# Optimization experiments

Measured on AMD Instinct MI355X. Metric: run time of the kernel, lower is better.

Reference implementation:

```python
import jax, jax.numpy as jnp
from jax import lax
import numpy as np

ROI = 7  # roi_size


def _extract_rois(feat, coords):
    """Faithful port of extract_roi_features: clamp a 7x7 window to image bounds,
    then bilinearly resize the (possibly smaller) crop back to 7x7
    (F.interpolate, mode='bilinear', align_corners=False)."""
    B, C, H, W = feat.shape
    half = ROI // 2

    def axis_idx(c, size):
        start = jnp.maximum(0, c - half)                  # [B,A]
        end = jnp.minimum(size, c + half + 1)
        Li = end - start                                  # crop length (int) [B,A]
        L = Li.astype(feat.dtype)[..., None]              # [B,A,1]
        j = jnp.arange(ROI, dtype=feat.dtype)
        # align_corners=False source coordinate, clamped into the crop
        src = jnp.clip((j + 0.5) * L / ROI - 0.5, 0.0, L - 1.0)  # [B,A,7]
        i0 = jnp.floor(src).astype(jnp.int32)
        i1 = jnp.minimum(i0 + 1, Li[..., None] - 1)
        w1 = src - i0.astype(feat.dtype)
        return start[..., None] + i0, start[..., None] + i1, 1.0 - w1, w1

    xc = coords[..., 0].astype(jnp.int32)
    yc = coords[..., 1].astype(jnp.int32)
    y0, y1, wy0, wy1 = axis_idx(yc, H)
    x0, x1, wx0, wx1 = axis_idx(xc, W)
    Bn, A = xc.shape
    bi = jnp.arange(Bn)[:, None, None, None]

    def g(Y, X):  # gather -> [B,A,7,7,C]
        return feat[bi, :, Y[:, :, :, None], X[:, :, None, :]]

    wy0 = wy0[:, :, :, None, None]; wy1 = wy1[:, :, :, None, None]
    wx0 = wx0[:, :, None, :, None]; wx1 = wx1[:, :, None, :, None]
    v = (wy0 * wx0 * g(y0, x0) + wy0 * wx1 * g(y0, x1)
         + wy1 * wx0 * g(y1, x0) + wy1 * wx1 * g(y1, x1))
    return jnp.transpose(v, (0, 1, 4, 2, 3))  # [B,A,C,7,7]


def _conv(x, w, b, pad):
    y = lax.conv_general_dilated(x, w, (1, 1), [(pad, pad), (pad, pad)],
                                 dimension_numbers=('NCHW', 'OIHW', 'NCHW'))
    return y + b[None, :, None, None]


def _bn(x, scale, bias, mean, var, eps=1e-5):
    inv = scale * lax.rsqrt(var + eps)
    return x * inv[None, :, None, None] + (bias - mean * inv)[None, :, None, None]


def setup_inputs() -> dict:
    key = jax.random.key(0)
    ks = jax.random.split(key, 12)
    B, A, C, H, W = 8, 128, 256, 64, 64
    f32 = jnp.float32
    d = {}
    d['feat_rgb'] = jax.random.normal(ks[0], (B, C, H, W), f32)
    d['feat_tir'] = jax.random.normal(ks[1], (B, C, H, W), f32)
    d['anchor_coords'] = jax.random.randint(ks[2], (B, A, 2), 0, 64).astype(jnp.int32)
    # local_fusion: Conv(2C->C,3) BN ReLU Conv(C->C,3) BN ReLU
    d['conv1_w'] = jax.random.normal(ks[3], (C, 2 * C, 3, 3), f32) * 0.02
    d['conv1_b'] = jnp.zeros((C,), f32)
    d['bn1_scale'] = jnp.ones((C,), f32)
    d['bn1_bias'] = jnp.zeros((C,), f32)
    d['bn1_mean'] = jax.random.normal(ks[4], (C,), f32) * 0.1
    d['bn1_var'] = jax.random.uniform(ks[5], (C,), f32, 0.5, 1.5)
    d['conv2_w'] = jax.random.normal(ks[6], (C, C, 3, 3), f32) * 0.02
    d['conv2_b'] = jnp.zeros((C,), f32)
    d['bn2_scale'] = jnp.ones((C,), f32)
    d['bn2_bias'] = jnp.zeros((C,), f32)
    d['bn2_mean'] = jax.random.normal(ks[7], (C,), f32) * 0.1
    d['bn2_var'] = jax.random.uniform(ks[8], (C,), f32, 0.5, 1.5)
    # weight_generator: Conv(C->C//4,1) ReLU Conv(C//4->2,1) Softmax(dim=1)
    d['wg1_w'] = jax.random.normal(ks[9], (C // 4, C, 1, 1), f32) * 0.05
    d['wg1_b'] = jnp.zeros((C // 4,), f32)
    d['wg2_w'] = jax.random.normal(ks[10], (2, C // 4, 1, 1), f32) * 0.05
    d['wg2_b'] = jnp.zeros((2,), f32)
    return d


def reference(feat_rgb, feat_tir, anchor_coords,
              conv1_w, conv1_b, bn1_scale, bn1_bias, bn1_mean, bn1_var,
              conv2_w, conv2_b, bn2_scale, bn2_bias, bn2_mean, bn2_var,
              wg1_w, wg1_b, wg2_w, wg2_b):
    B, C, H, W = feat_rgb.shape
    A = anchor_coords.shape[1]
    roi_rgb = _extract_rois(feat_rgb, anchor_coords)  # [B,A,C,7,7]
    roi_tir = _extract_rois(feat_tir, anchor_coords)
    rgb = roi_rgb.reshape(B * A, C, ROI, ROI)
    tir = roi_tir.reshape(B * A, C, ROI, ROI)
    x = jnp.concatenate([rgb, tir], axis=1)           # [B*A, 2C, 7, 7]
    x = jax.nn.relu(_bn(_conv(x, conv1_w, conv1_b, 1), bn1_scale, bn1_bias, bn1_mean, bn1_var))
    x = jax.nn.relu(_bn(_conv(x, conv2_w, conv2_b, 1), bn2_scale, bn2_bias, bn2_mean, bn2_var))
    h = jax.nn.relu(_conv(x, wg1_w, wg1_b, 0))
    w = jax.nn.softmax(_conv(h, wg2_w, wg2_b, 0), axis=1)  # [B*A, 2, 7, 7]
    fused = w[:, 0:1] * rgb + w[:, 1:2] * tir
    return fused.reshape(B, A, C, ROI, ROI)
```

## Files before the change

kernel.cpp:

```cpp
#include <hip/hip_runtime.h>
#include <cstddef>
#include <cstdint>


typedef unsigned int u32;
typedef unsigned short u16;
typedef __attribute__((ext_vector_type(8))) short short8;
typedef __attribute__((ext_vector_type(16))) float float16v;

__device__ __forceinline__ float bf2f(u16 u) {
  u32 x = ((u32)u) << 16;
  return __builtin_bit_cast(float, x);
}
__device__ __forceinline__ u16 f2bf(float f) {
  u32 x = __builtin_bit_cast(u32, f);
  x = x + 0x7fffu + ((x >> 16) & 1u);
  return (u16)(x >> 16);
}
__device__ __forceinline__ void gl_lds16(const void* g, void* l) {
  __builtin_amdgcn_global_load_lds((const __attribute__((address_space(1))) void*)g,
                                   (__attribute__((address_space(3))) void*)l, 16, 0, 0);
}

template <int IC>
__global__ void k_prep_w(const float* __restrict__ w, u16* __restrict__ wt) {
  int i = blockIdx.x * 256 + threadIdx.x;
  if (i >= 9 * 256 * IC) return;
  int e = i & 7;
  int r = i >> 3;
  int oc = r & 255;
  int r2 = r >> 8;
  int oct = r2 % (IC / 8);
  int t = r2 / (IC / 8);
  int ic = oct * 8 + e;
  wt[i] = f2bf(w[((size_t)oc * IC + ic) * 9 + t]);
}

__global__ void k_prep_bn(const float* __restrict__ cb, const float* __restrict__ sc,
                          const float* __restrict__ bi, const float* __restrict__ mn,
                          const float* __restrict__ vr, float* __restrict__ sb,
                          float* __restrict__ zp) {
  int c = threadIdx.x;
  float inv = sc[c] * rsqrtf(vr[c] + 1e-5f);
  sb[c]       = inv;
  sb[256 + c] = cb[c] * inv + (bi[c] - mn[c] * inv);
  zp[c] = 0.0f;
  zp[256 + c] = 0.0f;
}

__global__ __launch_bounds__(256)
void k_roi2(const float* __restrict__ frgb, const float* __restrict__ ftir,
            const int* __restrict__ coords, u16* __restrict__ cat) {
  int ba = blockIdx.x, b = ba >> 7, tid = threadIdx.x;
  __shared__ int   si0[2][7], si1[2][7];
  __shared__ float sw0[2][7], sw1[2][7];
  __shared__ u16 tile[49][514];
  if (tid < 14) {
    int axis = tid / 7;
    int j = tid - axis * 7;
    int c = coords[ba * 2 + (axis == 0 ? 1 : 0)];
    int start = max(0, c - 3);
    int end   = min(64, c + 4);
    int Li = end - start;
    float L = (float)Li;
    float src = ((float)j + 0.5f) * L / 7.0f - 0.5f;
    src = fminf(fmaxf(src, 0.0f), L - 1.0f);
    int i0 = (int)floorf(src);
    int i1 = min(i0 + 1, Li - 1);
    float w1 = src - (float)i0;
    si0[axis][j] = start + i0;
    si1[axis][j] = start + i1;
    sw0[axis][j] = 1.0f - w1;
    sw1[axis][j] = w1;
  }
  __syncthreads();
  const float* fr = frgb + (size_t)b * 256 * 4096;
  const float* ft = ftir + (size_t)b * 256 * 4096;
  for (int idx = tid; idx < 256 * 49; idx += 256) {
    int c = idx / 49, p = idx - c * 49;
    int jy = p / 7, jx = p - (p / 7) * 7;
    int y0 = si0[0][jy], y1 = si1[0][jy];
    int x0 = si0[1][jx], x1 = si1[1][jx];
    float wy0 = sw0[0][jy], wy1 = sw1[0][jy];
    float wx0 = sw0[1][jx], wx1 = sw1[1][jx];
    float a00 = wy0 * wx0, a01 = wy0 * wx1, a10 = wy1 * wx0, a11 = wy1 * wx1;
    const float* fc = fr + (size_t)c * 4096;
    float vr_ = a00 * fc[y0 * 64 + x0] + a01 * fc[y0 * 64 + x1] +
                a10 * fc[y1 * 64 + x0] + a11 * fc[y1 * 64 + x1];
    const float* gc = ft + (size_t)c * 4096;
    float vt_ = a00 * gc[y0 * 64 + x0] + a01 * gc[y0 * 64 + x1] +
                a10 * gc[y1 * 64 + x0] + a11 * gc[y1 * 64 + x1];
    tile[p][c]       = f2bf(vr_);
    tile[p][256 + c] = f2bf(vt_);
  }
  __syncthreads();
  u16* dst = cat + (size_t)ba * 49 * 512;
  for (int o = tid; o < 49 * 512; o += 256) {
    int row = o >> 9, c = o & 511;
    dst[o] = tile[row][c];
  }
}

template <int ICT, bool FIRST>
__global__ __launch_bounds__(1024, 4)
void k_conv_mfma(const u16* __restrict__ IN, const u16* __restrict__ WT,
                 const float* __restrict__ sb, const float* __restrict__ zpad,
                 u16* __restrict__ OUT) {
  constexpr int NC = ICT / 64;
  constexpr int BUFB = 208 * 128;
  __shared__ __align__(16) u16 lds[3][BUFB / 2];
  const int tid = threadIdx.x;
  const int lane = tid & 63, wv = tid >> 6;
  const int ng = wv & 3, mg = wv >> 2;
  const int l31 = lane & 31, h32 = lane >> 5;
  const int ba4 = blockIdx.x * 4;
  const char* inb = (const char*)IN;
  const char* zpb = (const char*)zpad;
  const bool dead1 = (mg == 3);

  int base_[2], qy_[2], qx_[2];
#pragma unroll
  for (int i = 0; i < 2; ++i) {
    int P = (mg + 4 * i) * 32 + l31;
    if (P > 195) P = 195;
    int roi = P / 49;
    int q = P - roi * 49;
    base_[i] = roi * 49;
    qy_[i] = q / 7;
    qx_[i] = q - (q / 7) * 7;
  }

  float16v acc[2][2];
#pragma unroll
  for (int i = 0; i < 2; ++i)
#pragma unroll
    for (int f = 0; f < 2; ++f)
#pragma unroll
      for (int e = 0; e < 16; ++e) acc[i][f][e] = 0.0f;

  auto stage = [&](int ch, int buf) {
    int cl = ((lane & 7) * 16) ^ (((lane >> 3) & 7) << 4);
#pragma unroll
    for (int u = 0; u < 2; ++u) {
      int s = wv + u * 16;
      int soff = (s <= 24) ? s * 1024 : 25 * 1024;
      int row_g = s * 8 + (lane >> 3);
      const char* src = (row_g < 196)
          ? (inb + ((size_t)(ba4 * 49 + row_g)) * (ICT * 2) + ch * 128 + cl)
          : (zpb + cl);
      gl_lds16(src, (char*)&lds[buf][0] + soff);
    }
  };

  const u16* wthr = WT + (size_t)h32 * 2048 + (size_t)(ng * 64 + l31) * 8;

  stage(0, 0);
  stage(1, 1);
  asm volatile("s_waitcnt vmcnt(2)" ::: "memory");
  __builtin_amdgcn_sched_barrier(0);
  __builtin_amdgcn_s_barrier();
  __builtin_amdgcn_sched_barrier(0);

#pragma unroll 1
  for (int ch = 0; ch < NC; ++ch) {
    if (ch + 2 < NC) stage(ch + 2, (ch + 2) % 3);
    const char* lb = (const char*)&lds[ch % 3][0];
    const u16* wch = wthr + (size_t)ch * 8 * 2048;

    short8 wfr[3][2];
#pragma unroll
    for (int jp = 0; jp < 2; ++jp)
#pragma unroll
      for (int f = 0; f < 2; ++f)
        wfr[jp][f] = *(const short8*)(
            wch + (size_t)(jp * 2) * 2048 + f * 256);
    int row0 = 0, row1 = 0;
#pragma unroll
    for (int j = 0; j < 36; ++j) {
      const int t = j >> 2, kk = j & 3;
      if (kk == 0) {
        const int dy = t / 3 - 1, dx = t - (t / 3) * 3 - 1;
#pragma unroll
        for (int i = 0; i < 2; ++i) {
          int iy = qy_[i] + dy, ix = qx_[i] + dx;
          int ok = ((u32)iy < 7u) & ((u32)ix < 7u);
          int row = ok ? (base_[i] + iy * 7 + ix) : 196;
          if (i == 0) row0 = row; else row1 = row;
        }
      }
      if (j + 2 < 36) {
        const int jn = j + 2;
#pragma unroll
        for (int f = 0; f < 2; ++f)
          wfr[jn % 3][f] = *(const short8*)(
              wch + (size_t)((jn >> 2) * (ICT / 8) + (jn & 3) * 2) * 2048 + f * 256);
      }
      short8 bfr[2];
      {
        int byt0 = row0 * 128 + ((kk * 32 + h32 * 16) ^ ((row0 & 7) << 4));
        bfr[0] = *(const short8*)(lb + byt0);
      }
      if (!dead1) {
        int byt1 = row1 * 128 + ((kk * 32 + h32 * 16) ^ ((row1 & 7) << 4));
        bfr[1] = *(const short8*)(lb + byt1);
      }
      __builtin_amdgcn_s_setprio(1);
#pragma unroll
      for (int i = 0; i < 2; ++i) {
        if (i == 1 && dead1) continue;
#pragma unroll
        for (int f = 0; f < 2; ++f)
          acc[i][f] = FIRST
              ? __builtin_amdgcn_mfma_f32_32x32x16_bf16(bfr[i], wfr[j % 3][f],
                                                        acc[i][f], 0, 0, 0)
              : __builtin_amdgcn_mfma_f32_32x32x16_bf16(wfr[j % 3][f], bfr[i],
                                                        acc[i][f], 0, 0, 0);
      }
      __builtin_amdgcn_s_setprio(0);
    }

    if (ch + 2 < NC) {
      asm volatile("s_waitcnt vmcnt(2)" ::: "memory");
    } else {
      asm volatile("s_waitcnt vmcnt(0)" ::: "memory");
    }
    __builtin_amdgcn_sched_barrier(0);
    __builtin_amdgcn_s_barrier();
    __builtin_amdgcn_sched_barrier(0);
  }

  if (FIRST) {
    u16* ob = OUT + (size_t)ba4 * 49 * 256;
#pragma unroll
    for (int f = 0; f < 2; ++f) {
      int oc = ng * 64 + f * 32 + l31;
      float s = sb[oc], bb = sb[256 + oc];
#pragma unroll
      for (int i = 0; i < 2; ++i) {
        if (i == 1 && dead1) continue;
        int ti = mg + 4 * i;
#pragma unroll
        for (int reg = 0; reg < 16; ++reg) {
          int m = (reg & 3) + 8 * (reg >> 2) + 4 * h32;
          int P = ti * 32 + m;
          if (P < 196)
            ob[(size_t)P * 256 + oc] = f2bf(fmaxf(acc[i][f][reg] * s + bb, 0.0f));
        }
      }
    }
  } else {
#pragma unroll
    for (int i = 0; i < 2; ++i) {
      if (i == 1 && dead1) continue;
      int ti = mg + 4 * i;
      int P = ti * 32 + l31;
      if (P < 196) {
        int roi = P / 49;
        int q = P - roi * 49;
        u16* ob = OUT + ((size_t)(ba4 + roi) * 256) * 49 + q;
#pragma unroll
        for (int f = 0; f < 2; ++f)
#pragma unroll
          for (int reg = 0; reg < 16; ++reg) {
            int oc = ng * 64 + f * 32 + (reg & 3) + 8 * (reg >> 2) + 4 * h32;
            float s = sb[oc], bb = sb[256 + oc];
            ob[(size_t)oc * 49] = f2bf(fmaxf(acc[i][f][reg] * s + bb, 0.0f));
          }
      }
    }
  }
}

__global__ __launch_bounds__(256)
void k_head_fuse(const u16* __restrict__ x3, const u16* __restrict__ cat,
                 const float* __restrict__ w1, const float* __restrict__ b1,
                 const float* __restrict__ w2, const float* __restrict__ b2,
                 float* __restrict__ out) {
  int ba  = blockIdx.x;
  int tid = threadIdx.x;
  __shared__ float xs[256 * 49];
  __shared__ float hs[64 * 49];
  __shared__ float ls[2 * 49];
  __shared__ float swx[2 * 49];
  const u16* src = x3 + (size_t)ba * 256 * 49;
  for (int idx = tid; idx < 256 * 49; idx += 256) xs[idx] = bf2f(src[idx]);
  __syncthreads();
  for (int idx = tid; idx < 64 * 49; idx += 256) {
    int oh = idx / 49, p = idx - oh * 49;
    float s = b1[oh];
    const float* wr = w1 + oh * 256;
    for (int ic = 0; ic < 256; ++ic) s += wr[ic] * xs[ic * 49 + p];
    hs[idx] = fmaxf(s, 0.0f);
  }
  __syncthreads();
  if (tid < 98) {
    int chn = tid / 49, p = tid - chn * 49;
    float s = b2[chn];
    const float* wr = w2 + chn * 64;
    for (int k = 0; k < 64; ++k) s += wr[k] * hs[k * 49 + p];
    ls[tid] = s;
  }
  __syncthreads();
  if (tid < 49) {
    float l0 = ls[tid], l1 = ls[49 + tid];
    float m = fmaxf(l0, l1);
    float e0 = expf(l0 - m), e1 = expf(l1 - m);
    float d = e0 + e1;
    swx[tid]      = e0 / d;
    swx[49 + tid] = e1 / d;
  }
  __syncthreads();
  const u16* cr = cat + (size_t)ba * 49 * 512;
  float* o = out + (size_t)ba * 256 * 49;
  for (int idx = tid; idx < 256 * 49; idx += 256) {
    int c = idx / 49, p = idx - (idx / 49) * 49;
    float rgb = bf2f(cr[p * 512 + c]);
    float tir = bf2f(cr[p * 512 + 256 + c]);
    o[idx] = swx[p] * rgb + swx[49 + p] * tir;
  }
}

extern "C" void kernel_launch(void* const* d_in, const int* in_sizes, int n_in,
                              void* d_out, int out_size, void* d_ws, size_t ws_size,
                              hipStream_t stream) {
  const float* feat_rgb = (const float*)d_in[0];
  const float* feat_tir = (const float*)d_in[1];
  const int*   coords   = (const int*)d_in[2];
  const float* conv1_w  = (const float*)d_in[3];
  const float* conv1_b  = (const float*)d_in[4];
  const float* bn1_s    = (const float*)d_in[5];
  const float* bn1_b    = (const float*)d_in[6];
  const float* bn1_m    = (const float*)d_in[7];
  const float* bn1_v    = (const float*)d_in[8];
  const float* conv2_w  = (const float*)d_in[9];
  const float* conv2_b  = (const float*)d_in[10];
  const float* bn2_s    = (const float*)d_in[11];
  const float* bn2_b    = (const float*)d_in[12];
  const float* bn2_m    = (const float*)d_in[13];
  const float* bn2_v    = (const float*)d_in[14];
  const float* wg1_w    = (const float*)d_in[15];
  const float* wg1_b    = (const float*)d_in[16];
  const float* wg2_w    = (const float*)d_in[17];
  const float* wg2_b    = (const float*)d_in[18];
  float* out = (float*)d_out;

  char* base = (char*)d_ws;
  u16*   W1T  = (u16*)(base);
  u16*   W2T  = (u16*)(base + 2359296);
  float* SB1  = (float*)(base + 3538944);
  float* SB2  = (float*)(base + 3540992);
  float* ZPAD = (float*)(base + 3543040);
  u16*   CAT  = (u16*)(base + 3545088);
  u16*   X2   = (u16*)(base + 3545088 + 51380224);
  u16*   X3   = (u16*)(base + 3545088 + 51380224 + 25690112);

  k_prep_w<512><<<(9 * 256 * 512 + 255) / 256, 256, 0, stream>>>(conv1_w, W1T);
  k_prep_w<256><<<(9 * 256 * 256 + 255) / 256, 256, 0, stream>>>(conv2_w, W2T);
  k_prep_bn<<<1, 256, 0, stream>>>(conv1_b, bn1_s, bn1_b, bn1_m, bn1_v, SB1, ZPAD);
  k_prep_bn<<<1, 256, 0, stream>>>(conv2_b, bn2_s, bn2_b, bn2_m, bn2_v, SB2, ZPAD);
  k_roi2<<<1024, 256, 0, stream>>>(feat_rgb, feat_tir, coords, CAT);
  k_conv_mfma<512, true><<<256, 1024, 0, stream>>>(CAT, W1T, SB1, ZPAD, X2);
  k_conv_mfma<256, false><<<256, 1024, 0, stream>>>(X2, W2T, SB2, ZPAD, X3);
  k_head_fuse<<<1024, 256, 0, stream>>>(X3, CAT, wg1_w, wg1_b, wg2_w, wg2_b, out);
}
```

Baseline: 674.0 us.

## Fuse both 3x3 convs into one kernel keeping intermediate activations in LDS

Merges the two conv MFMA kernels into one. The conv1 output for each block's 4 ROIs is written into a swizzled LDS buffer and conv2 reads it from there, so the X2 round trip through global memory and one launch are removed. Conv2 now writes X3 in position-major layout, and the head kernel's 1x1 conv is changed to read that layout. In exchange the staging pipeline drops from triple to double buffering with full __syncthreads, and the large LDS footprint (launch_bounds 1024,1) means one block per CU.

```diff
diff --git a/kernel.cpp b/kernel.cpp
--- a/kernel.cpp
+++ b/kernel.cpp
@@ -101,22 +101,28 @@
   }
 }
 
-template <int ICT, bool FIRST>
-__global__ __launch_bounds__(1024, 4)
-void k_conv_mfma(const u16* __restrict__ IN, const u16* __restrict__ WT,
-                 const float* __restrict__ sb, const float* __restrict__ zpad,
-                 u16* __restrict__ OUT) {
-  constexpr int NC = ICT / 64;
-  constexpr int BUFB = 208 * 128;
-  __shared__ __align__(16) u16 lds[3][BUFB / 2];
+__global__ __launch_bounds__(1024, 1)
+void k_conv_fused(const u16* __restrict__ CAT, const u16* __restrict__ W1T,
+                  const u16* __restrict__ W2T, const float* __restrict__ sb1,
+                  const float* __restrict__ sb2, const float* __restrict__ zpad,
+                  u16* __restrict__ X3) {
+  constexpr int NC1 = 8;
+  constexpr int NC2 = 4;
+  __shared__ __align__(16) u16 stg[2][208 * 64];
+  __shared__ __align__(16) u16 x2[200 * 256];
   const int tid = threadIdx.x;
   const int lane = tid & 63, wv = tid >> 6;
   const int ng = wv & 3, mg = wv >> 2;
   const int l31 = lane & 31, h32 = lane >> 5;
   const int ba4 = blockIdx.x * 4;
-  const char* inb = (const char*)IN;
+  const char* inb = (const char*)CAT;
   const char* zpb = (const char*)zpad;
   const bool dead1 = (mg == 3);
+
+  if (tid < 128) {
+    short8 zz = (short8){0, 0, 0, 0, 0, 0, 0, 0};
+    *(short8*)((char*)x2 + 196 * 512 + tid * 16) = zz;
+  }
 
   int base_[2], qy_[2], qx_[2];
 #pragma unroll
@@ -146,34 +152,29 @@
       int soff = (s <= 24) ? s * 1024 : 25 * 1024;
       int row_g = s * 8 + (lane >> 3);
       const char* src = (row_g < 196)
-          ? (inb + ((size_t)(ba4 * 49 + row_g)) * (ICT * 2) + ch * 128 + cl)
+          ? (inb + ((size_t)(ba4 * 49 + row_g)) * 1024 + ch * 128 + cl)
           : (zpb + cl);
-      gl_lds16(src, (char*)&lds[buf][0] + soff);
+      gl_lds16(src, (char*)&stg[buf][0] + soff);
     }
   };
 
-  const u16* wthr = WT + (size_t)h32 * 2048 + (size_t)(ng * 64 + l31) * 8;
+  const u16* wthr1 = W1T + (size_t)h32 * 2048 + (size_t)(ng * 64 + l31) * 8;
 
   stage(0, 0);
-  stage(1, 1);
-  asm volatile("s_waitcnt vmcnt(2)" ::: "memory");
-  __builtin_amdgcn_sched_barrier(0);
-  __builtin_amdgcn_s_barrier();
-  __builtin_amdgcn_sched_barrier(0);
+  __syncthreads();
 
 #pragma unroll 1
-  for (int ch = 0; ch < NC; ++ch) {
-    if (ch + 2 < NC) stage(ch + 2, (ch + 2) % 3);
-    const char* lb = (const char*)&lds[ch % 3][0];
-    const u16* wch = wthr + (size_t)ch * 8 * 2048;
+  for (int ch = 0; ch < NC1; ++ch) {
+    if (ch + 1 < NC1) stage(ch + 1, (ch + 1) & 1);
+    const char* lb = (const char*)&stg[ch & 1][0];
+    const u16* wch = wthr1 + (size_t)ch * 8 * 2048;
 
     short8 wfr[3][2];
 #pragma unroll
     for (int jp = 0; jp < 2; ++jp)
 #pragma unroll
       for (int f = 0; f < 2; ++f)
-        wfr[jp][f] = *(const short8*)(
-            wch + (size_t)(jp * 2) * 2048 + f * 256);
+        wfr[jp][f] = *(const short8*)(wch + (size_t)(jp * 2) * 2048 + f * 256);
     int row0 = 0, row1 = 0;
 #pragma unroll
     for (int j = 0; j < 36; ++j) {
@@ -193,7 +194,7 @@
 #pragma unroll
         for (int f = 0; f < 2; ++f)
           wfr[jn % 3][f] = *(const short8*)(
-              wch + (size_t)((jn >> 2) * (ICT / 8) + (jn & 3) * 2) * 2048 + f * 256);
+              wch + (size_t)((jn >> 2) * 64 + (jn & 3) * 2) * 2048 + f * 256);
       }
       short8 bfr[2];
       {
@@ -210,62 +211,111 @@
         if (i == 1 && dead1) continue;
 #pragma unroll
         for (int f = 0; f < 2; ++f)
-          acc[i][f] = FIRST
-              ? __builtin_amdgcn_mfma_f32_32x32x16_bf16(bfr[i], wfr[j % 3][f],
-                                                        acc[i][f], 0, 0, 0)
-              : __builtin_amdgcn_mfma_f32_32x32x16_bf16(wfr[j % 3][f], bfr[i],
-                                                        acc[i][f], 0, 0, 0);
+          acc[i][f] = __builtin_amdgcn_mfma_f32_32x32x16_bf16(
+              bfr[i], wfr[j % 3][f], acc[i][f], 0, 0, 0);
       }
       __builtin_amdgcn_s_setprio(0);
     }
-
-    if (ch + 2 < NC) {
-      asm volatile("s_waitcnt vmcnt(2)" ::: "memory");
-    } else {
-      asm volatile("s_waitcnt vmcnt(0)" ::: "memory");
-    }
-    __builtin_amdgcn_sched_barrier(0);
-    __builtin_amdgcn_s_barrier();
-    __builtin_amdgcn_sched_barrier(0);
-  }
-
-  if (FIRST) {
-    u16* ob = OUT + (size_t)ba4 * 49 * 256;
-#pragma unroll
-    for (int f = 0; f < 2; ++f) {
-      int oc = ng * 64 + f * 32 + l31;
-      float s = sb[oc], bb = sb[256 + oc];
-#pragma unroll
-      for (int i = 0; i < 2; ++i) {
-        if (i == 1 && dead1) continue;
-        int ti = mg + 4 * i;
-#pragma unroll
-        for (int reg = 0; reg < 16; ++reg) {
-          int m = (reg & 3) + 8 * (reg >> 2) + 4 * h32;
-          int P = ti * 32 + m;
-          if (P < 196)
-            ob[(size_t)P * 256 + oc] = f2bf(fmaxf(acc[i][f][reg] * s + bb, 0.0f));
-        }
-      }
-    }
-  } else {
+    __syncthreads();
+  }
+
+#pragma unroll
+  for (int f = 0; f < 2; ++f) {
+    int oc = ng * 64 + f * 32 + l31;
+    float s = sb1[oc], bb = sb1[256 + oc];
 #pragma unroll
     for (int i = 0; i < 2; ++i) {
       if (i == 1 && dead1) continue;
       int ti = mg + 4 * i;
-      int P = ti * 32 + l31;
-      if (P < 196) {
-        int roi = P / 49;
-        int q = P - roi * 49;
-        u16* ob = OUT + ((size_t)(ba4 + roi) * 256) * 49 + q;
+#pragma unroll
+      for (int reg = 0; reg < 16; ++reg) {
+        int m = (reg & 3) + 8 * (reg >> 2) + 4 * h32;
+        int P = ti * 32 + m;
+        if (P < 196)
+          x2[P * 256 + (oc ^ ((P & 7) << 3))] =
+              f2bf(fmaxf(acc[i][f][reg] * s + bb, 0.0f));
+      }
+    }
+  }
+  __syncthreads();
+
+#pragma unroll
+  for (int i = 0; i < 2; ++i)
+#pragma unroll
+    for (int f = 0; f < 2; ++f)
+#pragma unroll
+      for (int e = 0; e < 16; ++e) acc[i][f][e] = 0.0f;
+
+  const u16* wthr2 = W2T + (size_t)h32 * 2048 + (size_t)(ng * 64 + l31) * 8;
+  const char* x2b = (const char*)x2;
+
+#pragma unroll 1
+  for (int ch = 0; ch < NC2; ++ch) {
+    const u16* wch = wthr2 + (size_t)ch * 8 * 2048;
+    short8 wfr[3][2];
+#pragma unroll
+    for (int jp = 0; jp < 2; ++jp)
+#pragma unroll
+      for (int f = 0; f < 2; ++f)
+        wfr[jp][f] = *(const short8*)(wch + (size_t)(jp * 2) * 2048 + f * 256);
+    int row0 = 0, row1 = 0;
+#pragma unroll
+    for (int j = 0; j < 36; ++j) {
+      const int t = j >> 2, kk = j & 3;
+      if (kk == 0) {
+        const int dy = t / 3 - 1, dx = t - (t / 3) * 3 - 1;
+#pragma unroll
+        for (int i = 0; i < 2; ++i) {
+          int iy = qy_[i] + dy, ix = qx_[i] + dx;
+          int ok = ((u32)iy < 7u) & ((u32)ix < 7u);
+          int row = ok ? (base_[i] + iy * 7 + ix) : 196;
+          if (i == 0) row0 = row; else row1 = row;
+        }
+      }
+      if (j + 2 < 36) {
+        const int jn = j + 2;
 #pragma unroll
         for (int f = 0; f < 2; ++f)
-#pragma unroll
-          for (int reg = 0; reg < 16; ++reg) {
-            int oc = ng * 64 + f * 32 + (reg & 3) + 8 * (reg >> 2) + 4 * h32;
-            float s = sb[oc], bb = sb[256 + oc];
-            ob[(size_t)oc * 49] = f2bf(fmaxf(acc[i][f][reg] * s + bb, 0.0f));
-          }
+          wfr[jn % 3][f] = *(const short8*)(
+              wch + (size_t)((jn >> 2) * 32 + (jn & 3) * 2) * 2048 + f * 256);
+      }
+      short8 bfr[2];
+      {
+        int byt0 = row0 * 512 + ((ch * 128 + kk * 32 + h32 * 16) ^ ((row0 & 7) << 4));
+        bfr[0] = *(const short8*)(x2b + byt0);
+      }
+      if (!dead1) {
+        int byt1 = row1 * 512 + ((ch * 128 + kk * 32 + h32 * 16) ^ ((row1 & 7) << 4));
+        bfr[1] = *(const short8*)(x2b + byt1);
+      }
+      __builtin_amdgcn_s_setprio(1);
+#pragma unroll
+      for (int i = 0; i < 2; ++i) {
+        if (i == 1 && dead1) continue;
+#pragma unroll
+        for (int f = 0; f < 2; ++f)
+          acc[i][f] = __builtin_amdgcn_mfma_f32_32x32x16_bf16(
+              bfr[i], wfr[j % 3][f], acc[i][f], 0, 0, 0);
+      }
+      __builtin_amdgcn_s_setprio(0);
+    }
+  }
+
+  u16* ob = X3 + (size_t)ba4 * 49 * 256;
+#pragma unroll
+  for (int f = 0; f < 2; ++f) {
+    int oc = ng * 64 + f * 32 + l31;
+    float s = sb2[oc], bb = sb2[256 + oc];
+#pragma unroll
+    for (int i = 0; i < 2; ++i) {
+      if (i == 1 && dead1) continue;
+      int ti = mg + 4 * i;
+#pragma unroll
+      for (int reg = 0; reg < 16; ++reg) {
+        int m = (reg & 3) + 8 * (reg >> 2) + 4 * h32;
+        int P = ti * 32 + m;
+        if (P < 196)
+          ob[(size_t)P * 256 + oc] = f2bf(fmaxf(acc[i][f][reg] * s + bb, 0.0f));
       }
     }
   }
@@ -278,18 +328,19 @@
                  float* __restrict__ out) {
   int ba  = blockIdx.x;
   int tid = threadIdx.x;
-  __shared__ float xs[256 * 49];
+  __shared__ float xs[49 * 256];
   __shared__ float hs[64 * 49];
   __shared__ float ls[2 * 49];
   __shared__ float swx[2 * 49];
-  const u16* src = x3 + (size_t)ba * 256 * 49;
-  for (int idx = tid; idx < 256 * 49; idx += 256) xs[idx] = bf2f(src[idx]);
+  const u16* src = x3 + (size_t)ba * 49 * 256;
+  for (int idx = tid; idx < 49 * 256; idx += 256) xs[idx] = bf2f(src[idx]);
   __syncthreads();
   for (int idx = tid; idx < 64 * 49; idx += 256) {
     int oh = idx / 49, p = idx - oh * 49;
     float s = b1[oh];
     const float* wr = w1 + oh * 256;
-    for (int ic = 0; ic < 256; ++ic) s += wr[ic] * xs[ic * 49 + p];
+    const float* xr = xs + p * 256;
+    for (int ic = 0; ic < 256; ++ic) s += wr[ic] * xr[ic];
     hs[idx] = fmaxf(s, 0.0f);
   }
   __syncthreads();
@@ -351,15 +402,13 @@
   float* SB2  = (float*)(base + 3540992);
   float* ZPAD = (float*)(base + 3543040);
   u16*   CAT  = (u16*)(base + 3545088);
-  u16*   X2   = (u16*)(base + 3545088 + 51380224);
-  u16*   X3   = (u16*)(base + 3545088 + 51380224 + 25690112);
+  u16*   X3   = (u16*)(base + 3545088 + 51380224);
 
   k_prep_w<512><<<(9 * 256 * 512 + 255) / 256, 256, 0, stream>>>(conv1_w, W1T);
   k_prep_w<256><<<(9 * 256 * 256 + 255) / 256, 256, 0, stream>>>(conv2_w, W2T);
   k_prep_bn<<<1, 256, 0, stream>>>(conv1_b, bn1_s, bn1_b, bn1_m, bn1_v, SB1, ZPAD);
   k_prep_bn<<<1, 256, 0, stream>>>(conv2_b, bn2_s, bn2_b, bn2_m, bn2_v, SB2, ZPAD);
   k_roi2<<<1024, 256, 0, stream>>>(feat_rgb, feat_tir, coords, CAT);
-  k_conv_mfma<512, true><<<256, 1024, 0, stream>>>(CAT, W1T, SB1, ZPAD, X2);
-  k_conv_mfma<256, false><<<256, 1024, 0, stream>>>(X2, W2T, SB2, ZPAD, X3);
+  k_conv_fused<<<256, 1024, 0, stream>>>(CAT, W1T, W2T, SB1, SB2, ZPAD, X3);
   k_head_fuse<<<1024, 256, 0, stream>>>(X3, CAT, wg1_w, wg1_b, wg2_w, wg2_b, out);
 }
```

Measured after the change: 859.8 us. 1.28x slower.
